# Kernel tuning notes

Hardware: AMD Instinct MI355X
Metric: run time of the kernel (lower is better)

The kernel has to match this reference:

```python
import jax, jax.numpy as jnp
import numpy as np

B, L, N = 64, 64, 32           # programs, statement trees per program, nodes per tree
V, E, C, H, OUT = 100000, 128, 128, 100, 104
MAX_DEPTH = 10


def setup_inputs() -> dict:
    key = jax.random.key(0)
    ks = jax.random.split(key, 14)
    rng = np.random.default_rng(0)
    num_trees = B * L
    T = num_trees * N
    # random trees: parent index < node index, depth capped at MAX_DEPTH
    par = np.zeros((num_trees, N), np.int64)
    lev = np.zeros((num_trees, N), np.int64)
    for i in range(1, N):
        p = rng.integers(0, i, size=num_trees)
        pl = lev[np.arange(num_trees), p]
        too_deep = pl + 1 > MAX_DEPTH
        p = np.where(too_deep, 0, p)
        lev[:, i] = np.where(too_deep, 1, pl + 1)
        par[:, i] = p
    base = (np.arange(num_trees) * N)[:, None]
    parent = jnp.asarray((par + base).reshape(-1))          # global parent index
    level = jnp.asarray(lev.reshape(-1))
    tree_id = jnp.asarray(np.repeat(np.arange(num_trees), N))
    node_ids = jax.random.randint(ks[0], (T,), 0, V)
    r = lambda k, shape, s=0.05: (jax.random.normal(k, shape) * s).astype(jnp.float32)
    return {
        'node_ids': node_ids, 'parent': parent, 'level': level, 'tree_id': tree_id,
        'emb': r(ks[1], (V, E), 1.0),
        'W_lin': r(ks[2], (E, C)), 'b_lin': r(ks[3], (C,)),
        'w_ih_f': r(ks[4], (3 * H, C)), 'w_hh_f': r(ks[5], (3 * H, H)),
        'b_ih_f': r(ks[6], (3 * H,)), 'b_hh_f': r(ks[7], (3 * H,)),
        'w_ih_b': r(ks[8], (3 * H, C)), 'w_hh_b': r(ks[9], (3 * H, H)),
        'b_ih_b': r(ks[10], (3 * H,)), 'b_hh_b': r(ks[11], (3 * H,)),
        'fc_w': r(ks[12], (2 * H, OUT)), 'fc_b': r(ks[13], (OUT,)),
    }


def _run_gru(xs, wih, whh, bih, bhh, reverse):
    # xs: [L, B, C]; torch GRU gate math
    def step(hprev, x):
        gi = x @ wih.T + bih
        gh = hprev @ whh.T + bhh
        ir, iz, inn = jnp.split(gi, 3, axis=-1)
        hr, hz, hn = jnp.split(gh, 3, axis=-1)
        rg = jax.nn.sigmoid(ir + hr)
        zg = jax.nn.sigmoid(iz + hz)
        ng = jnp.tanh(inn + rg * hn)
        hnew = (1.0 - zg) * ng + zg * hprev
        return hnew, hnew
    h0 = jnp.zeros((xs.shape[1], whh.shape[1]), xs.dtype)
    _, out = jax.lax.scan(step, h0, xs, reverse=reverse)
    return out  # [L, B, H]


def _forward(node_ids, parent, level, tree_id, emb, W_lin, b_lin,
             w_ih_f, w_hh_f, b_ih_f, b_hh_f, w_ih_b, w_hh_b, b_ih_b, b_hh_b,
             fc_w, fc_b):
    # per-node: h = W*emb(id) + b, then child-sum bottom-up by depth level
    h = emb[node_ids] @ W_lin + b_lin            # [T, C]
    for d in range(MAX_DEPTH, 0, -1):
        contrib = jnp.where((level == d)[:, None], h, 0.0)
        h = h.at[parent].add(contrib)
    # per-tree max pool over all node hidden states -> statement vectors
    stmt = jax.ops.segment_max(h, tree_id, num_segments=B * L)  # [B*L, C]
    xs = stmt.reshape(B, L, C).transpose(1, 0, 2)               # [L, B, C]
    out_f = _run_gru(xs, w_ih_f, w_hh_f, b_ih_f, b_hh_f, reverse=False)
    out_b = _run_gru(xs, w_ih_b, w_hh_b, b_ih_b, b_hh_b, reverse=True)
    gru_out = jnp.concatenate([out_f, out_b], axis=-1)          # [L, B, 2H]
    pooled = gru_out.max(axis=0)                                # [B, 2H]
    return pooled @ fc_w + fc_b                                 # [B, OUT]


def reference(node_ids, parent, level, tree_id, emb, W_lin, b_lin,
              w_ih_f, w_hh_f, b_ih_f, b_hh_f, w_ih_b, w_hh_b, b_ih_b, b_hh_b,
              fc_w, fc_b):
    return _forward(node_ids, parent, level, tree_id, emb, W_lin, b_lin,
                    w_ih_f, w_hh_f, b_ih_f, b_hh_f, w_ih_b, w_hh_b, b_ih_b, b_hh_b,
                    fc_w, fc_b)
```

## Files before the change

### kernel.cpp

```cpp
#include <hip/hip_runtime.h>

typedef _Float16 half8 __attribute__((ext_vector_type(8)));
typedef _Float16 half4v __attribute__((ext_vector_type(4)));
typedef float f32x4 __attribute__((ext_vector_type(4)));
typedef float f32x16 __attribute__((ext_vector_type(16)));

union H8 { half8 h; float4 f; };

#define EDIM 128
#define CDIM 128
#define HDIM 100
#define ODIM 104

#define OFF_WIH    32768u
#define OFF_WHH    204800u
#define OFF_BIASP  376832u
#define OFF_STMT   379904u
#define OFF_POOL   1428480u

__device__ inline f32x4 zero4() { f32x4 z = {0.f, 0.f, 0.f, 0.f}; return z; }

__device__ inline float fast_exp2(float x) {
  float r; asm("v_exp_f32 %0, %1" : "=v"(r) : "v"(x)); return r;
}
__device__ inline float fast_rcp(float x) {
  float r; asm("v_rcp_f32 %0, %1" : "=v"(r) : "v"(x)); return r;
}
__device__ inline float sigmoid_f(float x) {
  return fast_rcp(1.f + fast_exp2(x * -1.44269504f));
}
__device__ inline float tanh_f(float x) {
  float e = fast_exp2(x * 2.88539008f);
  return fmaf(fast_rcp(1.f + e), -2.f, 1.f);
}

#define HSWZ(row) ((((row) & 3) << 4) ^ (((row) & 12) << 3))

__global__ __launch_bounds__(256, 2) void astnn_tree(
    const int* __restrict__ node_ids, const int* __restrict__ parent,
    const float* __restrict__ emb, const float* __restrict__ W_lin,
    const float* __restrict__ b_lin,
    const float* __restrict__ wihf, const float* __restrict__ whhf,
    const float* __restrict__ bihf, const float* __restrict__ bhhf,
    const float* __restrict__ wihb, const float* __restrict__ whhb,
    const float* __restrict__ bihb, const float* __restrict__ bhhb,
    _Float16* __restrict__ wihfrag, _Float16* __restrict__ whhfrag,
    float* __restrict__ biasP, _Float16* __restrict__ stmt)
{
  __shared__ _Float16 ldsW[16384];
  __shared__ _Float16 ldsA[16384];
  __shared__ int ldsPar[128];
  __shared__ unsigned ldsAnc[128];

  const int t = threadIdx.x, blk = blockIdx.x;
  const int w = t >> 6, l = t & 63;

  if (blk < 87) {
    int gid = blk * 256 + t;
    if (gid < 10752) {
      int i = gid, ll = i & 63, kc = (i >> 6) & 3;
      int rest = i >> 8, nt = rest % 21, d = rest / 21;
      const float* wih = d ? wihb : wihf;
      int n = (nt << 4) + (ll & 15), s = n / 112, j = n - 112 * s;
      int kb = (kc << 5) + ((ll >> 4) << 3);
#pragma unroll
      for (int e = 0; e < 8; e++) {
        int k = kb + e;
        float v = (j < HDIM) ? wih[(s * HDIM + j) * CDIM + k] : 0.f;
        wihfrag[i * 8 + e] = (_Float16)v;
      }
    } else if (gid < 21504) {
      int i = gid - 10752, ll = i & 63, kc = (i >> 6) & 3;
      int rest = i >> 8, nt = rest % 21, d = rest / 21;
      const float* whh = d ? whhb : whhf;
      const float* bhh = d ? bhhb : bhhf;
      int n = (nt << 4) + (ll & 15), s = n / 112, j = n - 112 * s;
      int kb = (kc << 5) + ((ll >> 4) << 3);
#pragma unroll
      for (int e = 0; e < 8; e++) {
        int k = kb + e;
        float v = 0.f;
        if (j < HDIM) {
          if (k < HDIM) v = whh[(s * HDIM + j) * HDIM + k];
          else if (k == HDIM && s == 2) v = bhh[2 * HDIM + j];
        }
        whhfrag[i * 8 + e] = (_Float16)v;
      }
    } else {
      int i = gid - 21504, d = i / 384, col = i % 384, s = col >> 7, j = col & 127;
      const float* bih = d ? bihb : bihf;
      const float* bhh = d ? bhhb : bhhf;
      float v = 0.f;
      if (j < HDIM) { v = bih[s * HDIM + j]; if (s < 2) v += bhh[s * HDIM + j]; }
      biasP[i] = v;
    }
  }

  {
#pragma unroll
    for (int i8 = 0; i8 < 8; i8++) {
      int fi = i8 * 256 + t;
      int ll = fi & 63, kc = (fi >> 6) & 3, nt = fi >> 8;
      int n = (nt << 4) + (ll & 15);
      int kb = (kc << 5) + ((ll >> 4) << 3);
      H8 u;
#pragma unroll
      for (int e = 0; e < 8; e++)
        u.h[e] = (_Float16)W_lin[(kb + e) * CDIM + n];
      *(float4*)&ldsW[fi * 8] = u.f;
    }
  }

#pragma unroll 1
  for (int half = 0; half < 2; ++half) {
    const int base = (blk * 2 + half) * 128;

    if (t < 128) ldsPar[t] = parent[base + t] & 31;

    {
      const int r = t >> 1, hf = t & 1;
      const int nid = node_ids[base + r];
      const float4* erow = (const float4*)(emb + (size_t)nid * EDIM) + hf * 16;
#pragma unroll
      for (int b2 = 0; b2 < 2; b2++) {
        float4 stage[8];
#pragma unroll
        for (int i = 0; i < 8; i++) stage[i] = erow[b2 * 8 + i];
#pragma unroll
        for (int c4 = 0; c4 < 4; c4++) {
          H8 u;
#pragma unroll
          for (int e = 0; e < 8; e++)
            u.h[e] = (_Float16)(((const float*)&stage[0])[c4 * 8 + e]);
          int c = b2 * 4 + c4;
          int addr = (r * 256 + hf * 128 + c * 16) ^ ((r & 7) << 4);
          *(float4*)((char*)ldsA + addr) = u.f;
        }
      }
    }
    __syncthreads();

    f32x4 acc[2][8];
#pragma unroll
    for (int mt = 0; mt < 2; mt++)
#pragma unroll
      for (int nt = 0; nt < 8; nt++) acc[mt][nt] = zero4();
#pragma unroll
    for (int kc = 0; kc < 4; kc++) {
      half8 af[2];
#pragma unroll
      for (int mt = 0; mt < 2; mt++) {
        int row = (w * 2 + mt) * 16 + (l & 15);
        int addr = (row * 256 + (kc << 6) + ((l >> 4) << 4)) ^ ((row & 7) << 4);
        af[mt] = *(const half8*)((const char*)ldsA + addr);
      }
#pragma unroll
      for (int nt = 0; nt < 8; nt++) {
        half8 bf = *(const half8*)&ldsW[(((nt << 2) | kc) * 64 + l) * 8];
        acc[0][nt] = __builtin_amdgcn_mfma_f32_16x16x32_f16(af[0], bf, acc[0][nt], 0, 0, 0);
        acc[1][nt] = __builtin_amdgcn_mfma_f32_16x16x32_f16(af[1], bf, acc[1][nt], 0, 0, 0);
      }
    }
    if (t < 128) {
      int tree = t >> 5;
      unsigned mask = 0;
      int cur = t & 31;
#pragma unroll
      for (int it = 0; it < 11; ++it) { mask |= (1u << cur); cur = ldsPar[tree * 32 + cur]; }
      ldsAnc[t] = mask;
    }
    __syncthreads();

#pragma unroll
    for (int mt = 0; mt < 2; mt++) {
      const int Mt = w * 2 + mt, tree = Mt >> 1, kc2 = Mt & 1;
      const int ebase = ((l >> 4) & 1) << 2;
      const int l2hi = ((l >> 4) >> 1) << 5;
#pragma unroll
      for (int nt = 0; nt < 8; nt++) {
        const float bl = b_lin[nt * 16 + (l & 15)];
        const int nt2 = nt >> 1;
        const int ncol = ((nt & 1) << 4) + (l & 15);
        half4v v;
#pragma unroll
        for (int reg = 0; reg < 4; reg++)
          v[reg] = (_Float16)(acc[mt][nt][reg] + bl);
        int idx = (((((tree << 2) + nt2) << 1) + kc2) * 64 + (l2hi + ncol)) * 8 + ebase;
        *(half4v*)&ldsA[idx] = v;
      }
    }
    __syncthreads();

    {
      const int tree = w;
      half8 ancf[2];
#pragma unroll
      for (int kc2 = 0; kc2 < 2; kc2++) {
        H8 u;
#pragma unroll
        for (int e = 0; e < 8; e++) {
          int n = (kc2 << 4) + ((l >> 5) << 3) + e;
          unsigned m = ldsAnc[(tree << 5) + n];
          u.h[e] = (_Float16)(float)((m >> (l & 31)) & 1u);
        }
        ancf[kc2] = u.h;
      }
      f32x16 acc2[4];
#pragma unroll
      for (int nt2 = 0; nt2 < 4; nt2++)
#pragma unroll
        for (int e = 0; e < 16; e++) acc2[nt2][e] = 0.f;
#pragma unroll
      for (int nt2 = 0; nt2 < 4; nt2++)
#pragma unroll
        for (int kc2 = 0; kc2 < 2; kc2++) {
          half8 bf = *(const half8*)&ldsA[(((((tree << 2) + nt2) << 1) + kc2) * 64 + l) * 8];
          acc2[nt2] = __builtin_amdgcn_mfma_f32_32x32x16_f16(ancf[kc2], bf, acc2[nt2], 0, 0, 0);
        }
#pragma unroll
      for (int nt2 = 0; nt2 < 4; nt2++) {
        float m1 = acc2[nt2][0];
#pragma unroll
        for (int e = 1; e < 16; e++) m1 = fmaxf(m1, acc2[nt2][e]);
        m1 = fmaxf(m1, __shfl_xor(m1, 32));
        if (l < 32) {
          int g = (blk * 2 + half) * 4 + tree;
          int rowp = (g & 63) * 64 + (g >> 6);
          stmt[(size_t)rowp * CDIM + (nt2 << 5) + l] = (_Float16)m1;
        }
      }
    }
    __syncthreads();
  }
}

__global__ __launch_bounds__(448) void astnn_gru(
    const _Float16* __restrict__ whhfrag, const _Float16* __restrict__ wihfrag,
    const _Float16* __restrict__ stmt, const float* __restrict__ biasP,
    float* __restrict__ pooled)
{
  __shared__ _Float16 hlds[4096];
  const int t = threadIdx.x, w = t >> 6, l = t & 63;
  const int mb = blockIdx.x, dir = blockIdx.y;
  for (int i = t; i < 512; i += 448)
    ((float4*)hlds)[i] = make_float4(0.f, 0.f, 0.f, 0.f);
  __syncthreads();
  if (t < 32) {
    int row = t & 15, buf = t >> 4;
    int addr = ((row * 256 + 200) ^ HSWZ(row)) + (buf << 12);
    *(_Float16*)((char*)hlds + addr) = (_Float16)1.0f;
  }

  const int j = (w << 4) + (l & 15);
  const bool jv = (j < HDIM);
  const int rloc = (l >> 4) << 2;
  const int grow = (mb << 4) + rloc;

  int raddr[4], waddr[4];
  {
    int row = l & 15;
#pragma unroll
    for (int kc = 0; kc < 4; kc++)
      raddr[kc] = (row * 256 + (kc << 6) + ((l >> 4) << 4)) ^ HSWZ(row);
#pragma unroll
    for (int reg = 0; reg < 4; reg++) {
      int rw = rloc + reg;
      waddr[reg] = (rw * 256 + (j << 1)) ^ HSWZ(rw);
    }
  }

  half8 bfr[3][4], bfw[3][4];
  {
    const half8* wfh = (const half8*)whhfrag + dir * 5376;
    const half8* wfi = (const half8*)wihfrag + dir * 5376;
#pragma unroll
    for (int s = 0; s < 3; s++)
#pragma unroll
      for (int kc = 0; kc < 4; kc++) {
        int idx = (((s * 7 + w) << 2) + kc) * 64 + l;
        bfr[s][kc] = wfh[idx];
        bfw[s][kc] = wfi[idx];
      }
  }
  const float bias0 = biasP[dir * 384 + j];
  const float bias1 = biasP[dir * 384 + 128 + j];
  const float bias2 = biasP[dir * 384 + 256 + j];

  int soff[4];
#pragma unroll
  for (int kc = 0; kc < 4; kc++)
    soff[kc] = (((mb << 4) + (l & 15)) * 256) + (kc << 6) + ((l >> 4) << 4);
  const ptrdiff_t sstep = dir ? -16384 : 16384;
  const char* sbase = (const char*)stmt + (size_t)(dir ? 63 : 0) * 16384;

  half8 sfA[4], sfB[4];
#pragma unroll
  for (int kc = 0; kc < 4; kc++) sfA[kc] = *(const half8*)(sbase + soff[kc]);
  const char* spre = sbase + sstep;
#pragma unroll
  for (int kc = 0; kc < 4; kc++) sfB[kc] = *(const half8*)(spre + soff[kc]);
  spre += sstep;

  f32x4 giA[3], giB[3];
  giA[0] = f32x4{bias0, bias0, bias0, bias0};
  giA[1] = f32x4{bias1, bias1, bias1, bias1};
  giA[2] = f32x4{bias2, bias2, bias2, bias2};
#pragma unroll
  for (int kc = 0; kc < 4; kc++) {
    giA[0] = __builtin_amdgcn_mfma_f32_16x16x32_f16(sfA[kc], bfw[0][kc], giA[0], 0, 0, 0);
    giA[1] = __builtin_amdgcn_mfma_f32_16x16x32_f16(sfA[kc], bfw[1][kc], giA[1], 0, 0, 0);
    giA[2] = __builtin_amdgcn_mfma_f32_16x16x32_f16(sfA[kc], bfw[2][kc], giA[2], 0, 0, 0);
  }

  float hreg[4], pool[4];
#pragma unroll
  for (int i = 0; i < 4; i++) { hreg[i] = 0.f; pool[i] = -3.0e38f; }
  __syncthreads();

#define GRU_BODY(GIC, GIN, SFsrc, SFdst, ROFF, WOFF, CN, PF)                    \
  {                                                                             \
    half8 afh[4];                                                               \
    _Pragma("unroll")                                                           \
    for (int kc = 0; kc < 4; kc++)                                              \
      afh[kc] = *(const half8*)((const char*)hlds + raddr[kc] + (ROFF));        \
    f32x4 acc0 = GIC[0], acc1 = GIC[1];                                         \
    f32x4 acc2i = GIC[2], acc2h = zero4();                                      \
    _Pragma("unroll")                             \
    for (int kc = 0; kc < 4; kc++) {                                            \
      acc0  = __builtin_amdgcn_mfma_f32_16x16x32_f16(afh[kc], bfr[0][kc], acc0, 0, 0, 0); \
      acc1  = __builtin_amdgcn_mfma_f32_16x16x32_f16(afh[kc], bfr[1][kc], acc1, 0, 0, 0); \
      acc2h = __builtin_amdgcn_mfma_f32_16x16x32_f16(afh[kc], bfr[2][kc], acc2h, 0, 0, 0);\
    }                                                                           \
    if (CN) {     \
      GIN[0] = f32x4{bias0, bias0, bias0, bias0};                               \
      GIN[1] = f32x4{bias1, bias1, bias1, bias1};                               \
      GIN[2] = f32x4{bias2, bias2, bias2, bias2};                               \
      _Pragma("unroll")                                                         \
      for (int kc = 0; kc < 4; kc++) {                                          \
        GIN[0] = __builtin_amdgcn_mfma_f32_16x16x32_f16(SFsrc[kc], bfw[0][kc], GIN[0], 0, 0, 0); \
        GIN[1] = __builtin_amdgcn_mfma_f32_16x16x32_f16(SFsrc[kc], bfw[1][kc], GIN[1], 0, 0, 0); \
        GIN[2] = __builtin_amdgcn_mfma_f32_16x16x32_f16(SFsrc[kc], bfw[2][kc], GIN[2], 0, 0, 0); \
      }                                                                         \
    }                                                                           \
    if (PF) {                                                                   \
      SFdst[0] = *(const half8*)(spre + soff[0]);                               \
      SFdst[1] = *(const half8*)(spre + soff[1]);                               \
      SFdst[2] = *(const half8*)(spre + soff[2]);                               \
      SFdst[3] = *(const half8*)(spre + soff[3]);                               \
      spre += sstep;                                                            \
    }                                                                           \
    _Pragma("unroll")                                                           \
    for (int reg = 0; reg < 4; reg++) {                                         \
      float r = sigmoid_f(acc0[reg]);                                           \
      float z = sigmoid_f(acc1[reg]);                                           \
      float n = tanh_f(fmaf(r, acc2h[reg], acc2i[reg]));                        \
      float hn = n + z * (hreg[reg] - n);                                       \
      hreg[reg] = hn;                                                           \
      pool[reg] = fmaxf(pool[reg], hn);                                         \
      if (jv)                                                                   \
        *(_Float16*)((char*)hlds + waddr[reg] + (WOFF)) = (_Float16)hn;         \
    }                                                                           \
    asm volatile("s_waitcnt lgkmcnt(0)" ::: "memory");                          \
    __builtin_amdgcn_s_barrier();                                               \
    __builtin_amdgcn_sched_barrier(0);                                          \
  }

#pragma unroll 1
  for (int it = 0; it < 31; ++it) {
    GRU_BODY(giA, giB, sfB, sfA, 0, 4096, 1, 1)
    GRU_BODY(giB, giA, sfA, sfB, 4096, 0, 1, 1)
  }
  GRU_BODY(giA, giB, sfB, sfA, 0, 4096, 1, 0)
  GRU_BODY(giB, giA, sfA, sfB, 4096, 0, 0, 0)
#undef GRU_BODY

  if (jv) {
#pragma unroll
    for (int reg = 0; reg < 4; reg++)
      pooled[((size_t)dir << 13) + ((size_t)(grow + reg) << 7) + j] = pool[reg];
  }
}

__global__ __launch_bounds__(128) void astnn_fc(
    const float* __restrict__ pooled, const float* __restrict__ fc_w,
    const float* __restrict__ fc_b, float* __restrict__ out)
{
  __shared__ float p[200];
  const int b = blockIdx.x, t = threadIdx.x;
  for (int i = t; i < 200; i += 128) {
    int d = i / 100, jj = i - d * 100;
    p[i] = pooled[((size_t)d << 13) + (b << 7) + jj];
  }
  __syncthreads();
  if (t < ODIM) {
    float a = fc_b[t];
#pragma unroll 8
    for (int k = 0; k < 200; k++) a = fmaf(p[k], fc_w[k * ODIM + t], a);
    out[b * ODIM + t] = a;
  }
}

extern "C" void kernel_launch(void* const* d_in, const int* in_sizes, int n_in,
                              void* d_out, int out_size, void* d_ws, size_t ws_size,
                              hipStream_t stream)
{
  const int* node_ids = (const int*)d_in[0];
  const int* parent   = (const int*)d_in[1];
  const float* emb    = (const float*)d_in[4];
  const float* W_lin  = (const float*)d_in[5];
  const float* b_lin  = (const float*)d_in[6];
  const float* wihf   = (const float*)d_in[7];
  const float* whhf   = (const float*)d_in[8];
  const float* bihf   = (const float*)d_in[9];
  const float* bhhf   = (const float*)d_in[10];
  const float* wihb   = (const float*)d_in[11];
  const float* whhb   = (const float*)d_in[12];
  const float* bihb   = (const float*)d_in[13];
  const float* bhhb   = (const float*)d_in[14];
  const float* fc_w   = (const float*)d_in[15];
  const float* fc_b   = (const float*)d_in[16];

  char* ws = (char*)d_ws;
  _Float16* wihfrag = (_Float16*)(ws + OFF_WIH);
  _Float16* whhfrag = (_Float16*)(ws + OFF_WHH);
  float* biasP      = (float*)(ws + OFF_BIASP);
  _Float16* stmt    = (_Float16*)(ws + OFF_STMT);
  float* pooled     = (float*)(ws + OFF_POOL);
  float* out        = (float*)d_out;

  astnn_tree<<<512, 256, 0, stream>>>(node_ids, parent, emb, W_lin, b_lin,
                                      wihf, whhf, bihf, bhhf,
                                      wihb, whhb, bihb, bhhb,
                                      wihfrag, whhfrag, biasP, stmt);
  astnn_gru<<<dim3(4, 2), 448, 0, stream>>>(whhfrag, wihfrag, stmt, biasP, pooled);
  astnn_fc<<<64, 128, 0, stream>>>(pooled, fc_w, fc_b, out);
}
```

Before: 83.47 us.

## Halve per-iteration tile to 64 nodes and raise tree-kernel occupancy to 3 blocks

The tree kernel now handles 64 nodes (2 trees) per loop iteration over 4 iterations instead of 128 nodes over 2. This halves the activation LDS buffer and the per-wave accumulator registers. Launch bounds go from 2 to 3 blocks per CU to hide gather latency with more resident waves. The trade-off is more barriers and loop iterations per block, and the ancestor-matrix MFMA work is now split across waves by column half.

```diff
diff --git a/kernel.cpp b/kernel.cpp
--- a/kernel.cpp
+++ b/kernel.cpp
@@ -36,7 +36,7 @@
 
 #define HSWZ(row) ((((row) & 3) << 4) ^ (((row) & 12) << 3))
 
-__global__ __launch_bounds__(256, 2) void astnn_tree(
+__global__ __launch_bounds__(256, 3) void astnn_tree(
     const int* __restrict__ node_ids, const int* __restrict__ parent,
     const float* __restrict__ emb, const float* __restrict__ W_lin,
     const float* __restrict__ b_lin,
@@ -48,9 +48,9 @@
     float* __restrict__ biasP, _Float16* __restrict__ stmt)
 {
   __shared__ _Float16 ldsW[16384];
-  __shared__ _Float16 ldsA[16384];
-  __shared__ int ldsPar[128];
-  __shared__ unsigned ldsAnc[128];
+  __shared__ _Float16 ldsA[8192];
+  __shared__ int ldsPar[64];
+  __shared__ unsigned ldsAnc[64];
 
   const int t = threadIdx.x, blk = blockIdx.x;
   const int w = t >> 6, l = t & 63;
@@ -112,56 +112,47 @@
   }
 
 #pragma unroll 1
-  for (int half = 0; half < 2; ++half) {
-    const int base = (blk * 2 + half) * 128;
-
-    if (t < 128) ldsPar[t] = parent[base + t] & 31;
+  for (int half = 0; half < 4; ++half) {
+    const int ti = blk * 4 + half;
+    const int base = ti * 64;
+
+    if (t < 64) ldsPar[t] = parent[base + t] & 31;
 
     {
-      const int r = t >> 1, hf = t & 1;
+      const int r = t >> 2, q = t & 3;
       const int nid = node_ids[base + r];
-      const float4* erow = (const float4*)(emb + (size_t)nid * EDIM) + hf * 16;
-#pragma unroll
-      for (int b2 = 0; b2 < 2; b2++) {
-        float4 stage[8];
-#pragma unroll
-        for (int i = 0; i < 8; i++) stage[i] = erow[b2 * 8 + i];
-#pragma unroll
-        for (int c4 = 0; c4 < 4; c4++) {
-          H8 u;
-#pragma unroll
-          for (int e = 0; e < 8; e++)
-            u.h[e] = (_Float16)(((const float*)&stage[0])[c4 * 8 + e]);
-          int c = b2 * 4 + c4;
-          int addr = (r * 256 + hf * 128 + c * 16) ^ ((r & 7) << 4);
-          *(float4*)((char*)ldsA + addr) = u.f;
-        }
+      const float4* erow = (const float4*)(emb + (size_t)nid * EDIM) + q * 8;
+      float4 stage[8];
+#pragma unroll
+      for (int i = 0; i < 8; i++) stage[i] = erow[i];
+#pragma unroll
+      for (int c4 = 0; c4 < 4; c4++) {
+        H8 u;
+#pragma unroll
+        for (int e = 0; e < 8; e++)
+          u.h[e] = (_Float16)(((const float*)&stage[0])[c4 * 8 + e]);
+        int c = q * 4 + c4;
+        int addr = (r * 256 + c * 16) ^ ((r & 7) << 4);
+        *(float4*)((char*)ldsA + addr) = u.f;
       }
     }
     __syncthreads();
 
-    f32x4 acc[2][8];
-#pragma unroll
-    for (int mt = 0; mt < 2; mt++)
-#pragma unroll
-      for (int nt = 0; nt < 8; nt++) acc[mt][nt] = zero4();
+    f32x4 acc[8];
+#pragma unroll
+    for (int nt = 0; nt < 8; nt++) acc[nt] = zero4();
 #pragma unroll
     for (int kc = 0; kc < 4; kc++) {
-      half8 af[2];
-#pragma unroll
-      for (int mt = 0; mt < 2; mt++) {
-        int row = (w * 2 + mt) * 16 + (l & 15);
-        int addr = (row * 256 + (kc << 6) + ((l >> 4) << 4)) ^ ((row & 7) << 4);
-        af[mt] = *(const half8*)((const char*)ldsA + addr);
-      }
+      int row = (w << 4) + (l & 15);
+      int addr = (row * 256 + (kc << 6) + ((l >> 4) << 4)) ^ ((row & 7) << 4);
+      half8 af = *(const half8*)((const char*)ldsA + addr);
 #pragma unroll
       for (int nt = 0; nt < 8; nt++) {
         half8 bf = *(const half8*)&ldsW[(((nt << 2) | kc) * 64 + l) * 8];
-        acc[0][nt] = __builtin_amdgcn_mfma_f32_16x16x32_f16(af[0], bf, acc[0][nt], 0, 0, 0);
-        acc[1][nt] = __builtin_amdgcn_mfma_f32_16x16x32_f16(af[1], bf, acc[1][nt], 0, 0, 0);
-      }
-    }
-    if (t < 128) {
+        acc[nt] = __builtin_amdgcn_mfma_f32_16x16x32_f16(af, bf, acc[nt], 0, 0, 0);
+      }
+    }
+    if (t < 64) {
       int tree = t >> 5;
       unsigned mask = 0;
       int cur = t & 31;
@@ -171,9 +162,8 @@
     }
     __syncthreads();
 
-#pragma unroll
-    for (int mt = 0; mt < 2; mt++) {
-      const int Mt = w * 2 + mt, tree = Mt >> 1, kc2 = Mt & 1;
+    {
+      const int tree = w >> 1, kc2 = w & 1;
       const int ebase = ((l >> 4) & 1) << 2;
       const int l2hi = ((l >> 4) >> 1) << 5;
 #pragma unroll
@@ -184,7 +174,7 @@
         half4v v;
 #pragma unroll
         for (int reg = 0; reg < 4; reg++)
-          v[reg] = (_Float16)(acc[mt][nt][reg] + bl);
+          v[reg] = (_Float16)(acc[nt][reg] + bl);
         int idx = (((((tree << 2) + nt2) << 1) + kc2) * 64 + (l2hi + ncol)) * 8 + ebase;
         *(half4v*)&ldsA[idx] = v;
       }
@@ -192,7 +182,7 @@
     __syncthreads();
 
     {
-      const int tree = w;
+      const int tree = w & 1, nh = w >> 1;
       half8 ancf[2];
 #pragma unroll
       for (int kc2 = 0; kc2 < 2; kc2++) {
@@ -205,26 +195,29 @@
         }
         ancf[kc2] = u.h;
       }
-      f32x16 acc2[4];
-#pragma unroll
-      for (int nt2 = 0; nt2 < 4; nt2++)
-#pragma unroll
-        for (int e = 0; e < 16; e++) acc2[nt2][e] = 0.f;
-#pragma unroll
-      for (int nt2 = 0; nt2 < 4; nt2++)
+      f32x16 acc2[2];
+#pragma unroll
+      for (int i = 0; i < 2; i++)
+#pragma unroll
+        for (int e = 0; e < 16; e++) acc2[i][e] = 0.f;
+#pragma unroll
+      for (int i = 0; i < 2; i++) {
+        const int nt2 = nh * 2 + i;
 #pragma unroll
         for (int kc2 = 0; kc2 < 2; kc2++) {
           half8 bf = *(const half8*)&ldsA[(((((tree << 2) + nt2) << 1) + kc2) * 64 + l) * 8];
-          acc2[nt2] = __builtin_amdgcn_mfma_f32_32x32x16_f16(ancf[kc2], bf, acc2[nt2], 0, 0, 0);
+          acc2[i] = __builtin_amdgcn_mfma_f32_32x32x16_f16(ancf[kc2], bf, acc2[i], 0, 0, 0);
         }
-#pragma unroll
-      for (int nt2 = 0; nt2 < 4; nt2++) {
-        float m1 = acc2[nt2][0];
-#pragma unroll
-        for (int e = 1; e < 16; e++) m1 = fmaxf(m1, acc2[nt2][e]);
+      }
+#pragma unroll
+      for (int i = 0; i < 2; i++) {
+        const int nt2 = nh * 2 + i;
+        float m1 = acc2[i][0];
+#pragma unroll
+        for (int e = 1; e < 16; e++) m1 = fmaxf(m1, acc2[i][e]);
         m1 = fmaxf(m1, __shfl_xor(m1, 32));
         if (l < 32) {
-          int g = (blk * 2 + half) * 4 + tree;
+          int g = ti * 2 + tree;
           int rowp = (g & 63) * 64 + (g >> 6);
           stmt[(size_t)rowp * CDIM + (nt2 << 5) + l] = (_Float16)m1;
         }
```

After: 86.13 us. 1.03x slower.
